# Kernel tuning notes

Hardware: AMD Instinct MI355X
Metric: run time of the kernel (lower is better)

Reference implementation:

```python
import jax, jax.numpy as jnp
import numpy as np

HEAD_DIM = 64
EPS = 1e-06


def yat_dense(x, kernel, bias):
    # YatDense (nmn): y = (x.W)^2 / (||x - w||^2 + eps) * alpha_scale + b
    dot = x @ kernel                                  # [..., F]
    x_sq = jnp.sum(x * x, axis=-1, keepdims=True)     # [..., 1]
    w_sq = jnp.sum(kernel * kernel, axis=0)           # [F]
    dist = x_sq + w_sq - 2.0 * dot                    # squared euclidean distance
    y = (dot * dot) / (dist + EPS)
    feats = kernel.shape[1]
    scale = np.sqrt(feats) / np.log1p(feats)          # alpha=1 scaling
    return y * jnp.asarray(scale, x.dtype) + bias


def apply_rope(q, k):
    # q,k: [B,H,T,D]; interleaved-pair rotation, base 10000 (dim=HEAD_DIM)
    B, H, T, D = q.shape
    half = D // 2
    pos = jnp.arange(T, dtype=jnp.float32)
    freqs = 10000.0 ** (-jnp.arange(half, dtype=jnp.float32) / half)
    ang = pos[:, None] * freqs[None, :]               # [T, half]
    sin = jnp.sin(ang)[None, None, :, :, None]        # [1,1,T,half,1]
    cos = jnp.cos(ang)[None, None, :, :, None]

    def rot(t):
        ts = t.reshape(B, H, T, half, 2)
        t0, t1 = ts[..., 0:1], ts[..., 1:2]
        out = jnp.concatenate([t0 * cos - t1 * sin, t1 * cos + t0 * sin], axis=-1)
        return out.reshape(B, H, T, D)

    return rot(q), rot(k)


def setup_inputs() -> dict:
    key = jax.random.key(0)
    B, T, C, H = 2, 2048, 1024, 16
    k1, k2, k3, k4, k5 = jax.random.split(key, 5)
    x = jax.random.normal(k1, (B, T, C), dtype=jnp.float32)
    # causal mask, broadcast over batch
    mask = jnp.broadcast_to(jnp.tril(jnp.ones((T, T), dtype=bool))[None], (B, T, T))
    s = 1.0 / np.sqrt(C)
    w_attn = jax.random.normal(k2, (C, 3 * C), dtype=jnp.float32) * s
    b_attn = jnp.zeros((3 * C,), dtype=jnp.float32)
    w_proj = jax.random.normal(k3, (C, C), dtype=jnp.float32) * s
    b_proj = jnp.zeros((C,), dtype=jnp.float32)
    return {"x": x, "mask": mask, "w_attn": w_attn, "b_attn": b_attn,
            "w_proj": w_proj, "b_proj": b_proj}


def reference(x, mask, w_attn, b_attn, w_proj, b_proj):
    B, T, C = x.shape
    H = C // HEAD_DIM
    qkv = yat_dense(x, w_attn, b_attn)                     # [B,T,3C]
    qkv = qkv.reshape(B, T, 3, H, HEAD_DIM)
    q, k, v = jnp.moveaxis(qkv, 2, 0)                      # each [B,T,H,hd]
    q = jnp.swapaxes(q, 1, 2)                              # [B,H,T,hd]
    k = jnp.swapaxes(k, 1, 2)
    v = jnp.swapaxes(v, 1, 2)
    q, k = apply_rope(q, k)
    scale = jnp.asarray(np.sqrt(HEAD_DIM), x.dtype)
    attn = jnp.einsum('bhqd,bhkd->bhqk', q, k) / scale     # [B,H,T,T]
    neg = jnp.finfo(x.dtype).min
    attn = jnp.where(mask[:, None, :, :], attn, neg)
    attn = jax.nn.softmax(attn, axis=-1)
    out = jnp.einsum('bhqk,bhkd->bhqd', attn, v)           # [B,H,T,hd]
    out = jnp.swapaxes(out, 1, 2).reshape(B, T, C)
    return yat_dense(out, w_proj, b_proj)
```

## Files before the change

### kernel.cpp

```cpp
#include <hip/hip_runtime.h>
#include <hip/hip_bf16.h>
#include <cmath>

#define BB 2
#define TT 2048
#define CC 1024
#define HH 16
#define DD 64
#define ROWS (BB*TT)
#define N1 (3*CC)
#define EPS 1e-6f

using short8 = __attribute__((ext_vector_type(8))) short;
using f32x4  = __attribute__((ext_vector_type(4))) float;

__device__ __forceinline__ void gl_lds16(const __hip_bfloat16* g, unsigned short* l) {
    __builtin_amdgcn_global_load_lds(
        (const __attribute__((address_space(1))) unsigned int*)(g),
        (__attribute__((address_space(3))) unsigned int*)(l), 16, 0, 0);
}

__device__ __forceinline__ unsigned int bf16pair(float a, float b) {
    __hip_bfloat16 ha = (__hip_bfloat16)a, hb = (__hip_bfloat16)b;
    unsigned short ua = *(unsigned short*)&ha, ub = *(unsigned short*)&hb;
    return (unsigned int)ua | ((unsigned int)ub << 16);
}

__device__ __forceinline__ float bf2f(unsigned short u) {
    unsigned int v = (unsigned int)u << 16;
    return *(float*)&v;
}

__global__ void rope_init(float* __restrict__ rope,
                          float* __restrict__ wsqa, float* __restrict__ wsqp) {
    int idx = blockIdx.x * 256 + threadIdx.x;
    if (idx < N1) wsqa[idx] = 0.f;
    if (idx < CC) wsqp[idx] = 0.f;
    if (idx >= TT * 32) return;
    int t = idx >> 5, i = idx & 31;
    double freq = pow(10000.0, -(double)i / 32.0);
    float ang = (float)t * (float)freq;
    rope[idx * 2 + 0] = cosf(ang);
    rope[idx * 2 + 1] = sinf(ang);
}

__global__ void rowsq_cast(const float* __restrict__ X, float* __restrict__ xsq,
                           __hip_bfloat16* __restrict__ Xb, float* __restrict__ osq) {
    int row = blockIdx.x;
    int t = threadIdx.x;
    const float* xr = X + (size_t)row * CC;
    __hip_bfloat16* br = Xb + (size_t)row * CC;
    float p = 0.f;
#pragma unroll
    for (int i = 0; i < 4; ++i) {
        float v = xr[t + i * 256];
        p += v * v;
        br[t + i * 256] = (__hip_bfloat16)v;
    }
    __shared__ float s[256];
    s[t] = p;
    __syncthreads();
    for (int off = 128; off > 0; off >>= 1) {
        if (t < off) s[t] += s[t + off];
        __syncthreads();
    }
    if (t == 0) { xsq[row] = s[0]; osq[row] = 0.f; }
}

__global__ void transpose_colsq(const float* __restrict__ W,
                                __hip_bfloat16* __restrict__ Wt,
                                float* __restrict__ wsq, int K, int N) {
    __shared__ unsigned short tile[64][65];
    int n0 = blockIdx.x * 64, k0 = blockIdx.y * 64;
    int c = threadIdx.x & 63, rg = threadIdx.x >> 6;
    float part = 0.f;
#pragma unroll
    for (int rr = 0; rr < 16; ++rr) {
        int r = rg + rr * 4;
        float f = W[(size_t)(k0 + r) * N + n0 + c];
        __hip_bfloat16 h = (__hip_bfloat16)f;
        tile[r][c] = *(unsigned short*)&h;
        part += f * f;
    }
    atomicAdd(&wsq[n0 + c], part);
    __syncthreads();
#pragma unroll
    for (int rr = 0; rr < 16; ++rr) {
        int r = rg + rr * 4;
        unsigned short u = tile[c][r];
        Wt[(size_t)(n0 + r) * K + k0 + c] = *(__hip_bfloat16*)&u;
    }
}

template<int TM, int TN, typename OutT>
__global__ __launch_bounds__(256) void yat_gemm_big(
    const __hip_bfloat16* __restrict__ A,
    const __hip_bfloat16* __restrict__ Bt,
    const float* __restrict__ xsq, const float* __restrict__ wsq,
    const float* __restrict__ bias, OutT* __restrict__ C,
    int M, int N, int K, float scale) {
    constexpr int MT = TM / 32;
    constexpr int NT = TN / 32;
    constexpr int IA = TM / 64;
    constexpr int IB = TN / 64;
    __shared__ __align__(16) unsigned short As[TM * 32];
    __shared__ __align__(16) unsigned short Bs[TN * 32];
    int tid = threadIdx.x;
    int wave = tid >> 6, lane = tid & 63, quad = lane >> 4, l16 = lane & 15;
    int wr = wave >> 1, wc = wave & 1;
    int m0 = blockIdx.y * TM, n0 = blockIdx.x * TN;

    f32x4 acc[MT][NT];
#pragma unroll
    for (int mt = 0; mt < MT; ++mt)
#pragma unroll
        for (int nt = 0; nt < NT; ++nt) acc[mt][nt] = f32x4{0.f, 0.f, 0.f, 0.f};

    int lrow = lane >> 2, lk = (lane & 3) << 3;
    for (int k0 = 0; k0 < K; k0 += 32) {
        __syncthreads();
#pragma unroll
        for (int i = 0; i < IA; ++i)
            gl_lds16(A + (size_t)(m0 + (wave * IA + i) * 16 + lrow) * K + k0 + lk,
                     As + (wave * IA + i) * 512);
#pragma unroll
        for (int i = 0; i < IB; ++i)
            gl_lds16(Bt + (size_t)(n0 + (wave * IB + i) * 16 + lrow) * K + k0 + lk,
                     Bs + (wave * IB + i) * 512);
        __syncthreads();
        short8 af[MT], bf[NT];
#pragma unroll
        for (int mt = 0; mt < MT; ++mt)
            af[mt] = *(const short8*)(As + (wr * (TM / 2) + mt * 16 + l16) * 32 + quad * 8);
#pragma unroll
        for (int nt = 0; nt < NT; ++nt)
            bf[nt] = *(const short8*)(Bs + (wc * (TN / 2) + nt * 16 + l16) * 32 + quad * 8);
#pragma unroll
        for (int mt = 0; mt < MT; ++mt)
#pragma unroll
            for (int nt = 0; nt < NT; ++nt)
                acc[mt][nt] = __builtin_amdgcn_mfma_f32_16x16x32_bf16(af[mt], bf[nt], acc[mt][nt], 0, 0, 0);
    }
    int mb = m0 + wr * (TM / 2) + quad * 4;
#pragma unroll
    for (int nt = 0; nt < NT; ++nt) {
        int col = n0 + wc * (TN / 2) + nt * 16 + l16;
        float wq = wsq[col];
        float bs = bias[col];
#pragma unroll
        for (int mt = 0; mt < MT; ++mt) {
#pragma unroll
            for (int r = 0; r < 4; ++r) {
                int row = mb + mt * 16 + r;
                float dot = acc[mt][nt][r];
                float dist = xsq[row] + wq - 2.f * dot + EPS;
                C[(size_t)row * N + col] = (OutT)(dot * dot / dist * scale + bs);
            }
        }
    }
}

__global__ __launch_bounds__(256) void prep_qkv2(
    const unsigned short* __restrict__ qkvb, const float* __restrict__ rope,
    __hip_bfloat16* __restrict__ Qb, __hip_bfloat16* __restrict__ Kb,
    __hip_bfloat16* __restrict__ Vtb) {
    const float QSC = 0.125f * 1.44269504f;
    int t0 = blockIdx.x * 64;
    int h = blockIdx.y, b = blockIdx.z;
    int bh = b * HH + h;
    int tid = threadIdx.x;
    __shared__ unsigned short vt[64][72];
    int r = tid >> 2, g = tid & 3;
    int t = t0 + r;
    const unsigned short* base = qkvb + (size_t)(b * TT + t) * N1 + h * DD;
    const float* rp = rope + (size_t)t * 64;

    union U8 { uint4 v; unsigned short s[8]; };
    U8 qa, qb2, ka, kb2, va, vb2;
    qa.v  = *(const uint4*)(base + g * 16);
    qb2.v = *(const uint4*)(base + g * 16 + 8);
    ka.v  = *(const uint4*)(base + CC + g * 16);
    kb2.v = *(const uint4*)(base + CC + g * 16 + 8);
    va.v  = *(const uint4*)(base + 2 * CC + g * 16);
    vb2.v = *(const uint4*)(base + 2 * CC + g * 16 + 8);

    U8 qo0, qo1, ko0, ko1;
#pragma unroll
    for (int u = 0; u < 8; ++u) {
        int i = g * 8 + u;
        float cs = rp[2 * i], sn = rp[2 * i + 1];
        unsigned short uq0 = (u < 4) ? qa.s[2 * u] : qb2.s[2 * u - 8];
        unsigned short uq1 = (u < 4) ? qa.s[2 * u + 1] : qb2.s[2 * u - 7];
        unsigned short uk0 = (u < 4) ? ka.s[2 * u] : kb2.s[2 * u - 8];
        unsigned short uk1 = (u < 4) ? ka.s[2 * u + 1] : kb2.s[2 * u - 7];
        float q0 = bf2f(uq0), q1 = bf2f(uq1);
        float k0 = bf2f(uk0), k1 = bf2f(uk1);
        unsigned int qp = bf16pair((q0 * cs - q1 * sn) * QSC, (q1 * cs + q0 * sn) * QSC);
        unsigned int kp = bf16pair(k0 * cs - k1 * sn, k1 * cs + k0 * sn);
        if (u < 4) { ((unsigned int*)&qo0)[u] = qp; ((unsigned int*)&ko0)[u] = kp; }
        else       { ((unsigned int*)&qo1)[u - 4] = qp; ((unsigned int*)&ko1)[u - 4] = kp; }
    }
    __hip_bfloat16* qd = Qb + ((size_t)bh * TT + t) * DD + g * 16;
    __hip_bfloat16* kd = Kb + ((size_t)bh * TT + t) * DD + g * 16;
    *(uint4*)(qd) = qo0.v;  *(uint4*)(qd + 8) = qo1.v;
    *(uint4*)(kd) = ko0.v;  *(uint4*)(kd + 8) = ko1.v;

    *(uint4*)(&vt[r][g * 16]) = va.v;
    *(uint4*)(&vt[r][g * 16 + 8]) = vb2.v;
    __syncthreads();
#pragma unroll
    for (int p = 0; p < 2; ++p) {
        int d = (tid >> 3) + p * 32;
        int tl = (tid & 7) * 8;
        U8 w;
#pragma unroll
        for (int j = 0; j < 8; ++j) w.s[j] = vt[tl + j][d];
        *(uint4*)(Vtb + ((size_t)bh * DD + d) * TT + t0 + tl) = w.v;
    }
}

__global__ __launch_bounds__(256, 3) void attn_mfma6(
    const __hip_bfloat16* __restrict__ Qb, const __hip_bfloat16* __restrict__ Kb,
    const __hip_bfloat16* __restrict__ Vtb,
    __hip_bfloat16* __restrict__ out, float* __restrict__ osq) {
    int i = blockIdx.x;
    int xcd = i & 7;
    int r0 = i >> 3;
    int bh = xcd + 8 * (r0 & 3);
    int rr = r0 >> 2;
    int v = rr & 7, s = rr >> 3;
    int qblk = (s == 0) ? v : (s == 1) ? (15 - v) : (s == 2) ? (16 + v) : (31 - v);
    int b = bh >> 4, h = bh & 15;
    int tid = threadIdx.x;
    int wave = tid >> 6, lane = tid & 63, quad = lane >> 4, l16 = lane & 15;

    __shared__ __align__(16) unsigned short Ks[2][64 * 32];
    __shared__ __align__(16) unsigned short Vs[2][64 * 32];
    __shared__ __align__(16) unsigned short Ps[4][16 * 72];
    unsigned short* pp = &Ps[wave][0];

    const __hip_bfloat16* Qbase = Qb + (size_t)bh * TT * DD;
    const __hip_bfloat16* Kbase = Kb + (size_t)bh * TT * DD;
    const __hip_bfloat16* Vbase = Vtb + (size_t)bh * DD * TT;

    int qw = qblk * 64 + wave * 16;
    short8 qf0, qf1;
    {
        const __hip_bfloat16* qr = Qbase + (size_t)(qw + l16) * DD + quad * 8;
        qf0 = *(const short8*)(qr);
        qf1 = *(const short8*)(qr + 32);
    }
    short8 ones8;
#pragma unroll
    for (int u = 0; u < 8; ++u) ones8[u] = (short)0x3F80;

    f32x4 acc_o[4];
#pragma unroll
    for (int mt = 0; mt < 4; ++mt) acc_o[mt] = f32x4{0.f, 0.f, 0.f, 0.f};
    f32x4 acc_l = {0.f, 0.f, 0.f, 0.f};

    int srow = lane >> 2;
    int soff = (lane & 3) * 8;
    int q_g = qw + l16;

    for (int kt = 0; kt <= qblk; ++kt) {
        int k0 = kt * 64;
        __syncthreads();
        gl_lds16(Kbase + (size_t)(k0 + wave * 16 + srow) * DD + soff,      &Ks[0][wave * 512]);
        gl_lds16(Kbase + (size_t)(k0 + wave * 16 + srow) * DD + 32 + soff, &Ks[1][wave * 512]);
        gl_lds16(Vbase + (size_t)(wave * 16 + srow) * TT + k0 + soff,      &Vs[0][wave * 512]);
        gl_lds16(Vbase + (size_t)(wave * 16 + srow) * TT + k0 + 32 + soff, &Vs[1][wave * 512]);
        __syncthreads();

        f32x4 accs[4];
#pragma unroll
        for (int mt = 0; mt < 4; ++mt) {
            short8 kf0 = *(const short8*)(&Ks[0][(mt * 16 + l16) * 32 + quad * 8]);
            short8 kf1 = *(const short8*)(&Ks[1][(mt * 16 + l16) * 32 + quad * 8]);
            f32x4 z = {0.f, 0.f, 0.f, 0.f};
            z = __builtin_amdgcn_mfma_f32_16x16x32_bf16(kf0, qf0, z, 0, 0, 0);
            accs[mt] = __builtin_amdgcn_mfma_f32_16x16x32_bf16(kf1, qf1, z, 0, 0, 0);
        }
        int limit = (kt == qblk) ? q_g : 0x7FFFFFFF;
#pragma unroll
        for (int mt = 0; mt < 4; ++mt) {
            int keyb = k0 + mt * 16 + quad * 4;
            float p0 = exp2f(accs[mt][0]);
            float p1 = exp2f(accs[mt][1]);
            float p2 = exp2f(accs[mt][2]);
            float p3 = exp2f(accs[mt][3]);
            p0 = (keyb + 0 <= limit) ? p0 : 0.f;
            p1 = (keyb + 1 <= limit) ? p1 : 0.f;
            p2 = (keyb + 2 <= limit) ? p2 : 0.f;
            p3 = (keyb + 3 <= limit) ? p3 : 0.f;
            uint2 w2;
            w2.x = bf16pair(p0, p1);
            w2.y = bf16pair(p2, p3);
            *(uint2*)(pp + l16 * 72 + mt * 16 + quad * 4) = w2;
        }
        short8 pf0 = *(const short8*)(pp + l16 * 72 + quad * 8);
        short8 pf1 = *(const short8*)(pp + l16 * 72 + 32 + quad * 8);
#pragma unroll
        for (int mt = 0; mt < 4; ++mt) {
            short8 vf0 = *(const short8*)(&Vs[0][(mt * 16 + l16) * 32 + quad * 8]);
            short8 vf1 = *(const short8*)(&Vs[1][(mt * 16 + l16) * 32 + quad * 8]);
            acc_o[mt] = __builtin_amdgcn_mfma_f32_16x16x32_bf16(vf0, pf0, acc_o[mt], 0, 0, 0);
            acc_o[mt] = __builtin_amdgcn_mfma_f32_16x16x32_bf16(vf1, pf1, acc_o[mt], 0, 0, 0);
        }
        acc_l = __builtin_amdgcn_mfma_f32_16x16x32_bf16(ones8, pf0, acc_l, 0, 0, 0);
        acc_l = __builtin_amdgcn_mfma_f32_16x16x32_bf16(ones8, pf1, acc_l, 0, 0, 0);
    }
    float inv = 1.f / acc_l[0];
    float part = 0.f;
#pragma unroll
    for (int mt = 0; mt < 4; ++mt) {
        float o0 = acc_o[mt][0] * inv;
        float o1 = acc_o[mt][1] * inv;
        float o2 = acc_o[mt][2] * inv;
        float o3 = acc_o[mt][3] * inv;
        part += o0 * o0 + o1 * o1 + o2 * o2 + o3 * o3;
        uint2 w2;
        w2.x = bf16pair(o0, o1);
        w2.y = bf16pair(o2, o3);
        *(uint2*)(pp + l16 * 72 + mt * 16 + quad * 4) = w2;
    }
    part += __shfl_xor(part, 16, 64);
    part += __shfl_xor(part, 32, 64);
    if (quad == 0) atomicAdd(&osq[(size_t)b * TT + qw + l16], part);
    int rw = lane >> 2, cg = lane & 3;
    uint4 o0 = *(const uint4*)(pp + rw * 72 + cg * 16);
    uint4 o1 = *(const uint4*)(pp + rw * 72 + cg * 16 + 8);
    __hip_bfloat16* orow = out + (size_t)(b * TT + qw + rw) * CC + h * DD + cg * 16;
    *(uint4*)(orow) = o0;
    *(uint4*)(orow + 8) = o1;
}

extern "C" void kernel_launch(void* const* d_in, const int* in_sizes, int n_in,
                              void* d_out, int out_size, void* d_ws, size_t ws_size,
                              hipStream_t stream) {
    const float* x      = (const float*)d_in[0];
    const float* w_attn = (const float*)d_in[2];
    const float* b_attn = (const float*)d_in[3];
    const float* w_proj = (const float*)d_in[4];
    const float* b_proj = (const float*)d_in[5];
    float* out = (float*)d_out;

    char* ws = (char*)d_ws;
    __hip_bfloat16* qkvb = (__hip_bfloat16*)(ws + 0);
    __hip_bfloat16* xbf  = (__hip_bfloat16*)(ws + 25165824);
    __hip_bfloat16* aout = (__hip_bfloat16*)(ws + 33554432);
    __hip_bfloat16* watT = (__hip_bfloat16*)(ws + 41943040);
    __hip_bfloat16* wpT  = (__hip_bfloat16*)(ws + 48234496);
    float*          rope = (float*)(ws + 50331648);
    float*          xsq  = (float*)(ws + 50855936);
    float*          osq  = (float*)(ws + 50872320);
    float*          wsqa = (float*)(ws + 50888704);
    float*          wsqp = (float*)(ws + 50900992);
    __hip_bfloat16* Qb   = (__hip_bfloat16*)(ws + 50905088);
    __hip_bfloat16* Kb   = (__hip_bfloat16*)(ws + 59293696);
    __hip_bfloat16* Vtb  = (__hip_bfloat16*)(ws + 67682304);

    float scale1 = (float)(sqrt(3072.0) / log1p(3072.0));
    float scale2 = (float)(sqrt(1024.0) / log1p(1024.0));

    rope_init<<<256, 256, 0, stream>>>(rope, wsqa, wsqp);
    rowsq_cast<<<ROWS, 256, 0, stream>>>(x, xsq, xbf, osq);
    transpose_colsq<<<dim3(N1 / 64, CC / 64), 256, 0, stream>>>(w_attn, watT, wsqa, CC, N1);
    transpose_colsq<<<dim3(CC / 64, CC / 64), 256, 0, stream>>>(w_proj, wpT, wsqp, CC, CC);
    yat_gemm_big<128, 128, __hip_bfloat16><<<dim3(N1 / 128, ROWS / 128), 256, 0, stream>>>(
        xbf, watT, xsq, wsqa, b_attn, qkvb, ROWS, N1, CC, scale1);
    prep_qkv2<<<dim3(TT / 64, HH, BB), 256, 0, stream>>>(
        (const unsigned short*)qkvb, rope, Qb, Kb, Vtb);
    attn_mfma6<<<1024, 256, 0, stream>>>(Qb, Kb, Vtb, aout, osq);
    yat_gemm_big<128, 64, float><<<dim3(CC / 64, ROWS / 128), 256, 0, stream>>>(
        aout, wpT, osq, wsqp, b_proj, out, ROWS, CC, CC, scale2);
}
```

Measured before the change: 246.2 us.

## Fuse RoPE into QKV GEMM epilogue, merge prep kernels, use BK=64 GEMMs

The RoPE/scale step moves into the QKV GEMM epilogue, which writes Q and K straight into per-head layout (using a lane shuffle to pair elements). This removes the qkvb intermediate and most of prep_qkv2, and a small vtrans kernel now only transposes V. The rope/zero-init and row-square kernels are merged into one launch, as are the two weight transposes. Both GEMMs now load K=64 per barrier pair. The intent is fewer launches, less memory traffic and fewer syncs, at the cost of scattered 2-byte epilogue stores and an extra V buffer.

```diff
diff --git a/kernel.cpp b/kernel.cpp
--- a/kernel.cpp
+++ b/kernel.cpp
@@ -26,28 +26,26 @@
     return (unsigned int)ua | ((unsigned int)ub << 16);
 }
 
-__device__ __forceinline__ float bf2f(unsigned short u) {
-    unsigned int v = (unsigned int)u << 16;
-    return *(float*)&v;
-}
-
-__global__ void rope_init(float* __restrict__ rope,
-                          float* __restrict__ wsqa, float* __restrict__ wsqp) {
-    int idx = blockIdx.x * 256 + threadIdx.x;
-    if (idx < N1) wsqa[idx] = 0.f;
-    if (idx < CC) wsqp[idx] = 0.f;
-    if (idx >= TT * 32) return;
-    int t = idx >> 5, i = idx & 31;
-    double freq = pow(10000.0, -(double)i / 32.0);
-    float ang = (float)t * (float)freq;
-    rope[idx * 2 + 0] = cosf(ang);
-    rope[idx * 2 + 1] = sinf(ang);
-}
-
-__global__ void rowsq_cast(const float* __restrict__ X, float* __restrict__ xsq,
-                           __hip_bfloat16* __restrict__ Xb, float* __restrict__ osq) {
-    int row = blockIdx.x;
+__global__ void rope_rowsq(const float* __restrict__ X, float* __restrict__ xsq,
+                           __hip_bfloat16* __restrict__ Xb, float* __restrict__ osq,
+                           float* __restrict__ rope,
+                           float* __restrict__ wsqa, float* __restrict__ wsqp) {
+    int blk = blockIdx.x;
     int t = threadIdx.x;
+    if (blk >= ROWS) {
+        int idx = (blk - ROWS) * 256 + t;
+        if (idx < N1) wsqa[idx] = 0.f;
+        if (idx < CC) wsqp[idx] = 0.f;
+        if (idx < TT * 32) {
+            int tt = idx >> 5, i = idx & 31;
+            double freq = pow(10000.0, -(double)i / 32.0);
+            float ang = (float)tt * (float)freq;
+            rope[idx * 2 + 0] = cosf(ang);
+            rope[idx * 2 + 1] = sinf(ang);
+        }
+        return;
+    }
+    int row = blk;
     const float* xr = X + (size_t)row * CC;
     __hip_bfloat16* br = Xb + (size_t)row * CC;
     float p = 0.f;
@@ -67,9 +65,14 @@
     if (t == 0) { xsq[row] = s[0]; osq[row] = 0.f; }
 }
 
-__global__ void transpose_colsq(const float* __restrict__ W,
-                                __hip_bfloat16* __restrict__ Wt,
-                                float* __restrict__ wsq, int K, int N) {
+__global__ void transpose2(const float* __restrict__ Wa, __hip_bfloat16* __restrict__ WaT,
+                           float* __restrict__ wsqa,
+                           const float* __restrict__ Wp, __hip_bfloat16* __restrict__ WpT,
+                           float* __restrict__ wsqp) {
+    const float* W; __hip_bfloat16* Wt; float* wsq; int N;
+    if (blockIdx.z == 0) { W = Wa; Wt = WaT; wsq = wsqa; N = N1; }
+    else { if (blockIdx.x >= 16) return; W = Wp; Wt = WpT; wsq = wsqp; N = CC; }
+    const int K = CC;
     __shared__ unsigned short tile[64][65];
     int n0 = blockIdx.x * 64, k0 = blockIdx.y * 64;
     int c = threadIdx.x & 63, rg = threadIdx.x >> 6;
@@ -92,126 +95,124 @@
     }
 }
 
-template<int TM, int TN, typename OutT>
-__global__ __launch_bounds__(256) void yat_gemm_big(
+__global__ __launch_bounds__(256) void yat_gemm_qkv(
     const __hip_bfloat16* __restrict__ A,
     const __hip_bfloat16* __restrict__ Bt,
     const float* __restrict__ xsq, const float* __restrict__ wsq,
-    const float* __restrict__ bias, OutT* __restrict__ C,
-    int M, int N, int K, float scale) {
-    constexpr int MT = TM / 32;
-    constexpr int NT = TN / 32;
-    constexpr int IA = TM / 64;
-    constexpr int IB = TN / 64;
-    __shared__ __align__(16) unsigned short As[TM * 32];
-    __shared__ __align__(16) unsigned short Bs[TN * 32];
+    const float* __restrict__ bias, const float* __restrict__ rope,
+    __hip_bfloat16* __restrict__ Qb, __hip_bfloat16* __restrict__ Kb,
+    __hip_bfloat16* __restrict__ Vb, float scale) {
+    const int K = CC, N = N1;
+    __shared__ __align__(16) unsigned short As0[128 * 32], As1[128 * 32];
+    __shared__ __align__(16) unsigned short Bs0[128 * 32], Bs1[128 * 32];
     int tid = threadIdx.x;
     int wave = tid >> 6, lane = tid & 63, quad = lane >> 4, l16 = lane & 15;
     int wr = wave >> 1, wc = wave & 1;
-    int m0 = blockIdx.y * TM, n0 = blockIdx.x * TN;
-
-    f32x4 acc[MT][NT];
-#pragma unroll
-    for (int mt = 0; mt < MT; ++mt)
-#pragma unroll
-        for (int nt = 0; nt < NT; ++nt) acc[mt][nt] = f32x4{0.f, 0.f, 0.f, 0.f};
-
-    int lrow = lane >> 2, lk = (lane & 3) << 3;
-    for (int k0 = 0; k0 < K; k0 += 32) {
-        __syncthreads();
-#pragma unroll
-        for (int i = 0; i < IA; ++i)
-            gl_lds16(A + (size_t)(m0 + (wave * IA + i) * 16 + lrow) * K + k0 + lk,
-                     As + (wave * IA + i) * 512);
-#pragma unroll
-        for (int i = 0; i < IB; ++i)
-            gl_lds16(Bt + (size_t)(n0 + (wave * IB + i) * 16 + lrow) * K + k0 + lk,
-                     Bs + (wave * IB + i) * 512);
-        __syncthreads();
-        short8 af[MT], bf[NT];
-#pragma unroll
-        for (int mt = 0; mt < MT; ++mt)
-            af[mt] = *(const short8*)(As + (wr * (TM / 2) + mt * 16 + l16) * 32 + quad * 8);
-#pragma unroll
-        for (int nt = 0; nt < NT; ++nt)
-            bf[nt] = *(const short8*)(Bs + (wc * (TN / 2) + nt * 16 + l16) * 32 + quad * 8);
-#pragma unroll
-        for (int mt = 0; mt < MT; ++mt)
-#pragma unroll
-            for (int nt = 0; nt < NT; ++nt)
-                acc[mt][nt] = __builtin_amdgcn_mfma_f32_16x16x32_bf16(af[mt], bf[nt], acc[mt][nt], 0, 0, 0);
-    }
-    int mb = m0 + wr * (TM / 2) + quad * 4;
-#pragma unroll
-    for (int nt = 0; nt < NT; ++nt) {
-        int col = n0 + wc * (TN / 2) + nt * 16 + l16;
-        float wq = wsq[col];
-        float bs = bias[col];
-#pragma unroll
-        for (int mt = 0; mt < MT; ++mt) {
-#pragma unroll
-            for (int r = 0; r < 4; ++r) {
-                int row = mb + mt * 16 + r;
-                float dot = acc[mt][nt][r];
-                float dist = xsq[row] + wq - 2.f * dot + EPS;
-                C[(size_t)row * N + col] = (OutT)(dot * dot / dist * scale + bs);
+    int m0 = blockIdx.y * 128, n0 = blockIdx.x * 128;
+
+    f32x4 acc[4][4];
+#pragma unroll
+    for (int mt = 0; mt < 4; ++mt)
+#pragma unroll
+        for (int nt = 0; nt < 4; ++nt) acc[mt][nt] = f32x4{0.f, 0.f, 0.f, 0.f};
+
+    int srow = lane >> 2, soff = (lane & 3) << 3;
+    for (int k0 = 0; k0 < K; k0 += 64) {
+        __syncthreads();
+#pragma unroll
+        for (int i = 0; i < 2; ++i) {
+            int rowc = (wave * 2 + i) * 16;
+            const __hip_bfloat16* ap = A + (size_t)(m0 + rowc + srow) * K + k0 + soff;
+            gl_lds16(ap,      As0 + rowc * 32);
+            gl_lds16(ap + 32, As1 + rowc * 32);
+            const __hip_bfloat16* bp = Bt + (size_t)(n0 + rowc + srow) * K + k0 + soff;
+            gl_lds16(bp,      Bs0 + rowc * 32);
+            gl_lds16(bp + 32, Bs1 + rowc * 32);
+        }
+        __syncthreads();
+#pragma unroll
+        for (int h = 0; h < 2; ++h) {
+            const unsigned short* Ah = h ? As1 : As0;
+            const unsigned short* Bh = h ? Bs1 : Bs0;
+            short8 af[4], bf[4];
+#pragma unroll
+            for (int mt = 0; mt < 4; ++mt)
+                af[mt] = *(const short8*)(Ah + (wr * 64 + mt * 16 + l16) * 32 + quad * 8);
+#pragma unroll
+            for (int nt = 0; nt < 4; ++nt)
+                bf[nt] = *(const short8*)(Bh + (wc * 64 + nt * 16 + l16) * 32 + quad * 8);
+#pragma unroll
+            for (int mt = 0; mt < 4; ++mt)
+#pragma unroll
+                for (int nt = 0; nt < 4; ++nt)
+                    acc[mt][nt] = __builtin_amdgcn_mfma_f32_16x16x32_bf16(af[mt], bf[nt], acc[mt][nt], 0, 0, 0);
+        }
+    }
+    const float QSC = 0.125f * 1.44269504f;
+    int mb = m0 + wr * 64 + quad * 4;
+    int cbase = n0 + wc * 64;
+    int sec = n0 >> 10;
+    if (sec == 2) {
+#pragma unroll
+        for (int nt = 0; nt < 4; ++nt) {
+            int col = cbase + nt * 16 + l16;
+            float wq = wsq[col], bs = bias[col];
+            int h = (col & 1023) >> 6, d = col & 63;
+#pragma unroll
+            for (int mt = 0; mt < 4; ++mt) {
+#pragma unroll
+                for (int r = 0; r < 4; ++r) {
+                    int row = mb + mt * 16 + r;
+                    float dot = acc[mt][nt][r];
+                    float dist = xsq[row] + wq - 2.f * dot + EPS;
+                    float y = dot * dot / dist * scale + bs;
+                    int t = row & (TT - 1), bI = row >> 11;
+                    Vb[(((size_t)bI * HH + h) * TT + t) * DD + d] = (__hip_bfloat16)y;
+                }
             }
         }
-    }
-}
-
-__global__ __launch_bounds__(256) void prep_qkv2(
-    const unsigned short* __restrict__ qkvb, const float* __restrict__ rope,
-    __hip_bfloat16* __restrict__ Qb, __hip_bfloat16* __restrict__ Kb,
-    __hip_bfloat16* __restrict__ Vtb) {
-    const float QSC = 0.125f * 1.44269504f;
-    int t0 = blockIdx.x * 64;
-    int h = blockIdx.y, b = blockIdx.z;
-    int bh = b * HH + h;
-    int tid = threadIdx.x;
+    } else {
+        __hip_bfloat16* dst = sec ? Kb : Qb;
+        float sc = sec ? 1.f : QSC;
+#pragma unroll
+        for (int nt = 0; nt < 4; ++nt) {
+            int col = cbase + nt * 16 + l16;
+            float wq = wsq[col], bs = bias[col];
+            int h = (col & 1023) >> 6, d = col & 63;
+            int odd = l16 & 1;
+#pragma unroll
+            for (int mt = 0; mt < 4; ++mt) {
+#pragma unroll
+                for (int r = 0; r < 4; ++r) {
+                    int row = mb + mt * 16 + r;
+                    float dot = acc[mt][nt][r];
+                    float dist = xsq[row] + wq - 2.f * dot + EPS;
+                    float y = dot * dot / dist * scale + bs;
+                    float yp = __shfl_xor(y, 1, 64);
+                    int t = row & (TT - 1), bI = row >> 11;
+                    const float* rp = rope + (size_t)t * 64 + (d & 62);
+                    float cs = rp[0] * sc, sn = rp[1] * sc;
+                    float o = odd ? (y * cs + yp * sn) : (y * cs - yp * sn);
+                    dst[(((size_t)bI * HH + h) * TT + t) * DD + d] = (__hip_bfloat16)o;
+                }
+            }
+        }
+    }
+}
+
+__global__ __launch_bounds__(256) void vtrans(const unsigned short* __restrict__ Vb,
+                                              __hip_bfloat16* __restrict__ Vtb) {
+    int bh = blockIdx.y, t0 = blockIdx.x * 64, tid = threadIdx.x;
     __shared__ unsigned short vt[64][72];
-    int r = tid >> 2, g = tid & 3;
-    int t = t0 + r;
-    const unsigned short* base = qkvb + (size_t)(b * TT + t) * N1 + h * DD;
-    const float* rp = rope + (size_t)t * 64;
-
+    int r = tid >> 2, g = (tid & 3) * 16;
+    const unsigned short* src = Vb + ((size_t)bh * TT + t0 + r) * DD + g;
+    *(uint4*)&vt[r][g]     = *(const uint4*)src;
+    *(uint4*)&vt[r][g + 8] = *(const uint4*)(src + 8);
+    __syncthreads();
     union U8 { uint4 v; unsigned short s[8]; };
-    U8 qa, qb2, ka, kb2, va, vb2;
-    qa.v  = *(const uint4*)(base + g * 16);
-    qb2.v = *(const uint4*)(base + g * 16 + 8);
-    ka.v  = *(const uint4*)(base + CC + g * 16);
-    kb2.v = *(const uint4*)(base + CC + g * 16 + 8);
-    va.v  = *(const uint4*)(base + 2 * CC + g * 16);
-    vb2.v = *(const uint4*)(base + 2 * CC + g * 16 + 8);
-
-    U8 qo0, qo1, ko0, ko1;
-#pragma unroll
-    for (int u = 0; u < 8; ++u) {
-        int i = g * 8 + u;
-        float cs = rp[2 * i], sn = rp[2 * i + 1];
-        unsigned short uq0 = (u < 4) ? qa.s[2 * u] : qb2.s[2 * u - 8];
-        unsigned short uq1 = (u < 4) ? qa.s[2 * u + 1] : qb2.s[2 * u - 7];
-        unsigned short uk0 = (u < 4) ? ka.s[2 * u] : kb2.s[2 * u - 8];
-        unsigned short uk1 = (u < 4) ? ka.s[2 * u + 1] : kb2.s[2 * u - 7];
-        float q0 = bf2f(uq0), q1 = bf2f(uq1);
-        float k0 = bf2f(uk0), k1 = bf2f(uk1);
-        unsigned int qp = bf16pair((q0 * cs - q1 * sn) * QSC, (q1 * cs + q0 * sn) * QSC);
-        unsigned int kp = bf16pair(k0 * cs - k1 * sn, k1 * cs + k0 * sn);
-        if (u < 4) { ((unsigned int*)&qo0)[u] = qp; ((unsigned int*)&ko0)[u] = kp; }
-        else       { ((unsigned int*)&qo1)[u - 4] = qp; ((unsigned int*)&ko1)[u - 4] = kp; }
-    }
-    __hip_bfloat16* qd = Qb + ((size_t)bh * TT + t) * DD + g * 16;
-    __hip_bfloat16* kd = Kb + ((size_t)bh * TT + t) * DD + g * 16;
-    *(uint4*)(qd) = qo0.v;  *(uint4*)(qd + 8) = qo1.v;
-    *(uint4*)(kd) = ko0.v;  *(uint4*)(kd + 8) = ko1.v;
-
-    *(uint4*)(&vt[r][g * 16]) = va.v;
-    *(uint4*)(&vt[r][g * 16 + 8]) = vb2.v;
-    __syncthreads();
 #pragma unroll
     for (int p = 0; p < 2; ++p) {
-        int d = (tid >> 3) + p * 32;
-        int tl = (tid & 7) * 8;
+        int d = (tid >> 3) + p * 32, tl = (tid & 7) * 8;
         U8 w;
 #pragma unroll
         for (int j = 0; j < 8; ++j) w.s[j] = vt[tl + j][d];
@@ -228,8 +229,8 @@
     int r0 = i >> 3;
     int bh = xcd + 8 * (r0 & 3);
     int rr = r0 >> 2;
-    int v = rr & 7, s = rr >> 3;
-    int qblk = (s == 0) ? v : (s == 1) ? (15 - v) : (s == 2) ? (16 + v) : (31 - v);
+    int v = rr & 7, s2 = rr >> 3;
+    int qblk = (s2 == 0) ? v : (s2 == 1) ? (15 - v) : (s2 == 2) ? (16 + v) : (31 - v);
     int b = bh >> 4, h = bh & 15;
     int tid = threadIdx.x;
     int wave = tid >> 6, lane = tid & 63, quad = lane >> 4, l16 = lane & 15;
@@ -335,6 +336,87 @@
     *(uint4*)(orow + 8) = o1;
 }
 
+template<int TM, int TN, typename OutT>
+__global__ __launch_bounds__(256) void yat_gemm_bk64(
+    const __hip_bfloat16* __restrict__ A,
+    const __hip_bfloat16* __restrict__ Bt,
+    const float* __restrict__ xsq, const float* __restrict__ wsq,
+    const float* __restrict__ bias, OutT* __restrict__ C,
+    int M, int N, int K, float scale) {
+    constexpr int MT = TM / 32;
+    constexpr int NT = TN / 32;
+    constexpr int IA = TM / 64;
+    constexpr int IB = TN / 64;
+    __shared__ __align__(16) unsigned short As0[TM * 32];
+    __shared__ __align__(16) unsigned short As1[TM * 32];
+    __shared__ __align__(16) unsigned short Bs0[TN * 32];
+    __shared__ __align__(16) unsigned short Bs1[TN * 32];
+    int tid = threadIdx.x;
+    int wave = tid >> 6, lane = tid & 63, quad = lane >> 4, l16 = lane & 15;
+    int wr = wave >> 1, wc = wave & 1;
+    int m0 = blockIdx.y * TM, n0 = blockIdx.x * TN;
+
+    f32x4 acc[MT][NT];
+#pragma unroll
+    for (int mt = 0; mt < MT; ++mt)
+#pragma unroll
+        for (int nt = 0; nt < NT; ++nt) acc[mt][nt] = f32x4{0.f, 0.f, 0.f, 0.f};
+
+    int srow = lane >> 2, soff = (lane & 3) << 3;
+    for (int k0 = 0; k0 < K; k0 += 64) {
+        __syncthreads();
+#pragma unroll
+        for (int i = 0; i < IA; ++i) {
+            int rowc = (wave * IA + i) * 16;
+            const __hip_bfloat16* ap = A + (size_t)(m0 + rowc + srow) * K + k0 + soff;
+            gl_lds16(ap,      As0 + rowc * 32);
+            gl_lds16(ap + 32, As1 + rowc * 32);
+        }
+#pragma unroll
+        for (int i = 0; i < IB; ++i) {
+            int rowc = (wave * IB + i) * 16;
+            const __hip_bfloat16* bp = Bt + (size_t)(n0 + rowc + srow) * K + k0 + soff;
+            gl_lds16(bp,      Bs0 + rowc * 32);
+            gl_lds16(bp + 32, Bs1 + rowc * 32);
+        }
+        __syncthreads();
+#pragma unroll
+        for (int h = 0; h < 2; ++h) {
+            const unsigned short* Ah = h ? As1 : As0;
+            const unsigned short* Bh = h ? Bs1 : Bs0;
+            short8 af[MT], bf[NT];
+#pragma unroll
+            for (int mt = 0; mt < MT; ++mt)
+                af[mt] = *(const short8*)(Ah + (wr * (TM / 2) + mt * 16 + l16) * 32 + quad * 8);
+#pragma unroll
+            for (int nt = 0; nt < NT; ++nt)
+                bf[nt] = *(const short8*)(Bh + (wc * (TN / 2) + nt * 16 + l16) * 32 + quad * 8);
+#pragma unroll
+            for (int mt = 0; mt < MT; ++mt)
+#pragma unroll
+                for (int nt = 0; nt < NT; ++nt)
+                    acc[mt][nt] = __builtin_amdgcn_mfma_f32_16x16x32_bf16(af[mt], bf[nt], acc[mt][nt], 0, 0, 0);
+        }
+    }
+    int mb = m0 + wr * (TM / 2) + quad * 4;
+#pragma unroll
+    for (int nt = 0; nt < NT; ++nt) {
+        int col = n0 + wc * (TN / 2) + nt * 16 + l16;
+        float wq = wsq[col];
+        float bs = bias[col];
+#pragma unroll
+        for (int mt = 0; mt < MT; ++mt) {
+#pragma unroll
+            for (int r = 0; r < 4; ++r) {
+                int row = mb + mt * 16 + r;
+                float dot = acc[mt][nt][r];
+                float dist = xsq[row] + wq - 2.f * dot + EPS;
+                C[(size_t)row * N + col] = (OutT)(dot * dot / dist * scale + bs);
+            }
+        }
+    }
+}
+
 extern "C" void kernel_launch(void* const* d_in, const int* in_sizes, int n_in,
                               void* d_out, int out_size, void* d_ws, size_t ws_size,
                               hipStream_t stream) {
@@ -346,32 +428,29 @@
     float* out = (float*)d_out;
 
     char* ws = (char*)d_ws;
-    __hip_bfloat16* qkvb = (__hip_bfloat16*)(ws + 0);
-    __hip_bfloat16* xbf  = (__hip_bfloat16*)(ws + 25165824);
-    __hip_bfloat16* aout = (__hip_bfloat16*)(ws + 33554432);
-    __hip_bfloat16* watT = (__hip_bfloat16*)(ws + 41943040);
-    __hip_bfloat16* wpT  = (__hip_bfloat16*)(ws + 48234496);
-    float*          rope = (float*)(ws + 50331648);
-    float*          xsq  = (float*)(ws + 50855936);
-    float*          osq  = (float*)(ws + 50872320);
-    float*          wsqa = (float*)(ws + 50888704);
-    float*          wsqp = (float*)(ws + 50900992);
-    __hip_bfloat16* Qb   = (__hip_bfloat16*)(ws + 50905088);
-    __hip_bfloat16* Kb   = (__hip_bfloat16*)(ws + 59293696);
-    __hip_bfloat16* Vtb  = (__hip_bfloat16*)(ws + 67682304);
+    __hip_bfloat16* xbf  = (__hip_bfloat16*)(ws + 0);
+    __hip_bfloat16* aout = (__hip_bfloat16*)(ws + 8388608);
+    __hip_bfloat16* watT = (__hip_bfloat16*)(ws + 16777216);
+    __hip_bfloat16* wpT  = (__hip_bfloat16*)(ws + 23068672);
+    float*          rope = (float*)(ws + 25165824);
+    float*          xsq  = (float*)(ws + 25690112);
+    float*          osq  = (float*)(ws + 25706496);
+    float*          wsqa = (float*)(ws + 25722880);
+    float*          wsqp = (float*)(ws + 25735168);
+    __hip_bfloat16* Qb   = (__hip_bfloat16*)(ws + 25739264);
+    __hip_bfloat16* Kb   = (__hip_bfloat16*)(ws + 34127872);
+    __hip_bfloat16* Vb   = (__hip_bfloat16*)(ws + 42516480);
+    __hip_bfloat16* Vtb  = (__hip_bfloat16*)(ws + 50905088);
 
     float scale1 = (float)(sqrt(3072.0) / log1p(3072.0));
     float scale2 = (float)(sqrt(1024.0) / log1p(1024.0));
 
-    rope_init<<<256, 256, 0, stream>>>(rope, wsqa, wsqp);
-    rowsq_cast<<<ROWS, 256, 0, stream>>>(x, xsq, xbf, osq);
-    transpose_colsq<<<dim3(N1 / 64, CC / 64), 256, 0, stream>>>(w_attn, watT, wsqa, CC, N1);
-    transpose_colsq<<<dim3(CC / 64, CC / 64), 256, 0, stream>>>(w_proj, wpT, wsqp, CC, CC);
-    yat_gemm_big<128, 128, __hip_bfloat16><<<dim3(N1 / 128, ROWS / 128), 256, 0, stream>>>(
-        xbf, watT, xsq, wsqa, b_attn, qkvb, ROWS, N1, CC, scale1);
-    prep_qkv2<<<dim3(TT / 64, HH, BB), 256, 0, stream>>>(
-        (const unsigned short*)qkvb, rope, Qb, Kb, Vtb);
+    rope_rowsq<<<ROWS + 256, 256, 0, stream>>>(x, xsq, xbf, osq, rope, wsqa, wsqp);
+    transpose2<<<dim3(48, 16, 2), 256, 0, stream>>>(w_attn, watT, wsqa, w_proj, wpT, wsqp);
+    yat_gemm_qkv<<<dim3(N1 / 128, ROWS / 128), 256, 0, stream>>>(
+        xbf, watT, xsq, wsqa, b_attn, rope, Qb, Kb, Vb, scale1);
+    vtrans<<<dim3(TT / 64, BB * HH), 256, 0, stream>>>((const unsigned short*)Vb, Vtb);
     attn_mfma6<<<1024, 256, 0, stream>>>(Qb, Kb, Vtb, aout, osq);
-    yat_gemm_big<128, 64, float><<<dim3(CC / 64, ROWS / 128), 256, 0, stream>>>(
+    yat_gemm_bk64<128, 64, float><<<dim3(CC / 64, ROWS / 128), 256, 0, stream>>>(
         aout, wpT, osq, wsqp, b_proj, out, ROWS, CC, CC, scale2);
 }
```

Result: no change. 246.8 us (+0.2%).
